# Performance work log

Hardware: AMD Instinct MI355X
Metric: run time of the kernel (lower is better)

Reference implementation:

```python
import jax, jax.numpy as jnp
import numpy as np

D_MODEL = 1024
NHEADS = 16
E_HEAD = D_MODEL // NHEADS  # 64
ROPE_BASE = 10000.0


def _rope_cos_sin(L, dim, base, dtype):
    # dim = E_head (even); inv_freq over pairs, GPT-NeoX half-split convention
    inv_freq = 1.0 / (base ** (jnp.arange(0, dim, 2, dtype=jnp.float32) / dim))
    pos = jnp.arange(L, dtype=jnp.float32)
    freqs = pos[:, None] * inv_freq[None, :]  # [L, dim/2]
    return jnp.cos(freqs).astype(dtype), jnp.sin(freqs).astype(dtype)


def _apply_rope(t, cos, sin):
    # t: [B, H, L, Dh]; rotate-half formulation
    d2 = t.shape[-1] // 2
    t1, t2 = t[..., :d2], t[..., d2:]
    return jnp.concatenate([t1 * cos - t2 * sin, t1 * sin + t2 * cos], axis=-1)


def setup_inputs() -> dict:
    key = jax.random.key(0)
    ks = jax.random.split(key, 5)
    B, L = 4, 2048
    x = jax.random.normal(ks[0], (B, L, D_MODEL), dtype=jnp.float32)
    s_in = 1.0 / np.sqrt(D_MODEL)
    W_packed = jax.random.normal(ks[1], (3 * D_MODEL, D_MODEL), dtype=jnp.float32) * s_in
    b_packed = jax.random.normal(ks[2], (3 * D_MODEL,), dtype=jnp.float32) * 0.02
    W_out = jax.random.normal(ks[3], (D_MODEL, D_MODEL), dtype=jnp.float32) * s_in
    b_out = jax.random.normal(ks[4], (D_MODEL,), dtype=jnp.float32) * 0.02
    return {"x": x, "W_packed": W_packed, "b_packed": b_packed, "W_out": W_out, "b_out": b_out}


def reference(x, W_packed, b_packed, W_out, b_out):
    B, L, _ = x.shape
    # 1) packed QKV projection (query is key is value path)
    qkv = jnp.einsum('ble,fe->blf', x, W_packed) + b_packed  # [B, L, 3*D]
    q, k, v = jnp.split(qkv, 3, axis=-1)
    # 2) split heads -> [B, H, L, Dh]
    def heads(t):
        return t.reshape(B, L, NHEADS, E_HEAD).transpose(0, 2, 1, 3)
    q, k, v = heads(q), heads(k), heads(v)
    # 3) RoPE on q, k
    cos, sin = _rope_cos_sin(L, E_HEAD, ROPE_BASE, x.dtype)
    q = _apply_rope(q, cos, sin)
    k = _apply_rope(k, cos, sin)
    # 4) SDPA (non-causal, no dropout)
    scale = 1.0 / np.sqrt(E_HEAD)
    scores = jnp.einsum('bhqd,bhkd->bhqk', q, k) * scale
    attn = jax.nn.softmax(scores, axis=-1)
    out = jnp.einsum('bhqk,bhkd->bhqd', attn, v)
    # 5) merge heads + output projection
    out = out.transpose(0, 2, 1, 3).reshape(B, L, D_MODEL)
    return jnp.einsum('bld,ed->ble', out, W_out) + b_out
```

## Files before the change

kernel.cpp:

```cpp
#include <hip/hip_runtime.h>
#include <hip/hip_bf16.h>
#include <stdint.h>

#define L_SEQ 2048
#define NB    4
#define NH    16
#define EH    64
#define DM    1024
#define MTOT  (NB * L_SEQ)

typedef __attribute__((ext_vector_type(8))) short bf16x8;
typedef __attribute__((ext_vector_type(4))) float f32x4;
typedef __attribute__((ext_vector_type(16))) float f32x16;

static __device__ __forceinline__ float bf2f(short u) {
    union { unsigned int i; float f; } c;
    c.i = ((unsigned int)(unsigned short)u) << 16;
    return c.f;
}
static __device__ __forceinline__ short f2bf(float f) {
    union { float f; unsigned int i; } c; c.f = f;
    unsigned int x = c.i;
    unsigned int r = (x + 0x7fffu + ((x >> 16) & 1u)) >> 16;
    return (short)(unsigned short)r;
}
static __device__ __forceinline__ unsigned cvtpk(float lo, float hi) {
    unsigned r;
    asm volatile("v_cvt_pk_bf16_f32 %0, %1, %2" : "=v"(r) : "v"(lo), "v"(hi));
    return r;
}

static __device__ __forceinline__ void gload_lds16(const void* g, void* lds) {
    __builtin_amdgcn_global_load_lds(
        (const __attribute__((address_space(1))) unsigned int*)g,
        (__attribute__((address_space(3))) unsigned int*)lds, 16, 0, 0);
}

__global__ __launch_bounds__(256) void cvt3_k(const float* __restrict__ x,
                                              const float* __restrict__ wp,
                                              const float* __restrict__ wo,
                                              short* __restrict__ xb,
                                              short* __restrict__ wpb,
                                              short* __restrict__ wob,
                                              float* __restrict__ tab,
                                              float* __restrict__ tabT) {
    int bid = blockIdx.x;
    if (bid >= 12544) {
        int i = (bid - 12544) * 256 + threadIdx.x;
        int di = i >> 11, l = i & 2047;
        float inv = powf(10000.0f, -(float)di * (1.0f / 32.0f));
        float fr = (float)l * inv;
        tabT[i]         = cosf(fr);
        tabT[65536 + i] = sinf(fr);
        return;
    }
    if (bid >= 12288) {
        int i = (bid - 12288) * 256 + threadIdx.x;
        int l = i >> 5, d = i & 31;
        float inv = powf(10000.0f, -(float)d * (1.0f / 32.0f));
        float fr = (float)l * inv;
        tab[i]         = cosf(fr);
        tab[65536 + i] = sinf(fr);
        return;
    }
    const float* src; short* dst; int i;
    if (bid < 8192)       { src = x;  dst = xb;  i = bid * 256 + threadIdx.x; }
    else if (bid < 11264) { src = wp; dst = wpb; i = (bid - 8192) * 256 + threadIdx.x; }
    else                  { src = wo; dst = wob; i = (bid - 11264) * 256 + threadIdx.x; }
    float4 v = ((const float4*)src)[i];
    short4 o;
    o.x = f2bf(v.x); o.y = f2bf(v.y); o.z = f2bf(v.z); o.w = f2bf(v.w);
    ((short4*)dst)[i] = o;
}

template<int OUTBF16, int NBN, int NCOL, int EPI>
__global__ __launch_bounds__(512, 2) void gemmA_k(const short* __restrict__ A,
                                                  const short* __restrict__ Bt,
                                                  const float* __restrict__ bias,
                                                  void* __restrict__ Cv,
                                                  short* __restrict__ Qp,
                                                  short* __restrict__ Kp,
                                                  short* __restrict__ Vt) {
    __shared__ short lds[2][384 * 32];
    const int t = threadIdx.x;
    const int w = t >> 6, l = t & 63;
    const int wm = w >> 1, wn = w & 1;
    const int lr = l & 15, lh = l >> 4;

    const int nblk = NBN * 32;
    int fid = blockIdx.x + blockIdx.y * NBN;
    int swz = (fid & 7) * (nblk >> 3) + (fid >> 3);
    const int n0 = (swz % NBN) * 128;
    const int m0 = (swz / NBN) * 256;

    const int lrow = l >> 2;
    const int schunk = (l & 3) ^ ((l >> 3) & 3);

    const short* Ag = A + (size_t)(m0 + lrow) * 1024 + schunk * 8;
    const short* Bg = Bt + (size_t)(n0 + lrow) * 1024 + schunk * 8;

    auto STAGE = [&](int kt, int buf) {
        gload_lds16(Ag + (size_t)(w * 32) * 1024 + kt * 32,      &lds[buf][(w * 32) * 32]);
        gload_lds16(Ag + (size_t)(w * 32 + 16) * 1024 + kt * 32, &lds[buf][(w * 32 + 16) * 32]);
        gload_lds16(Bg + (size_t)(w * 16) * 1024 + kt * 32,      &lds[buf][8192 + (w * 16) * 32]);
    };

    f32x4 acc[4][4] = {};

    STAGE(0, 0);
    STAGE(1, 1);
    asm volatile("s_waitcnt vmcnt(3)" ::: "memory");
    __builtin_amdgcn_s_barrier();

    const int fch = (lh ^ ((lr >> 1) & 3)) << 3;

#pragma unroll 2
    for (int kt = 0; kt < 32; ++kt) {
        const int c = kt & 1;
        const short* Al = &lds[c][0];
        const short* Bl = &lds[c][8192];

        bf16x8 bfr[4], af[4];
#pragma unroll
        for (int nj = 0; nj < 4; ++nj)
            bfr[nj] = *(const bf16x8*)(Bl + (wn * 64 + nj * 16 + lr) * 32 + fch);
#pragma unroll
        for (int mi = 0; mi < 4; ++mi)
            af[mi] = *(const bf16x8*)(Al + (wm * 64 + mi * 16 + lr) * 32 + fch);

        __builtin_amdgcn_s_setprio(1);
#pragma unroll
        for (int mi = 0; mi < 4; ++mi)
#pragma unroll
            for (int nj = 0; nj < 4; ++nj)
                acc[mi][nj] = __builtin_amdgcn_mfma_f32_16x16x32_bf16(
                    af[mi], bfr[nj], acc[mi][nj], 0, 0, 0);
        __builtin_amdgcn_s_setprio(0);

        asm volatile("s_waitcnt lgkmcnt(0)" ::: "memory");
        __builtin_amdgcn_s_barrier();
        if (kt + 2 < 32) {
            STAGE(kt + 2, c);
            asm volatile("s_waitcnt vmcnt(3)" ::: "memory");
        } else {
            asm volatile("s_waitcnt vmcnt(0)" ::: "memory");
        }
        __builtin_amdgcn_s_barrier();
    }

    if (EPI == 0) {
#pragma unroll
        for (int mi = 0; mi < 4; ++mi) {
#pragma unroll
            for (int nj = 0; nj < 4; ++nj) {
                const int row = m0 + wm * 64 + mi * 16 + lh * 4;
                const int col = n0 + wn * 64 + nj * 16 + lr;
                const float bsv = bias[col];
#pragma unroll
                for (int j = 0; j < 4; ++j) {
                    float v = acc[mi][nj][j] + bsv;
                    if (OUTBF16)
                        ((short*)Cv)[(size_t)(row + j) * NCOL + col] = f2bf(v);
                    else
                        ((float*)Cv)[(size_t)(row + j) * NCOL + col] = v;
                }
            }
        }
    } else {
        const int part = n0 >> 10;
        const int h = ((n0 & 1023) >> 6) + wn;
#pragma unroll
        for (int mi = 0; mi < 4; ++mi) {
            const int r0 = m0 + wm * 64 + mi * 16 + lh * 4;
            const int bq = r0 >> 11, lq = r0 & 2047;
            if (part < 2) {
                short* Drow = (part == 0 ? Qp : Kp) + ((size_t)(bq * 16 + h) * 2048 + lq) * 64;
#pragma unroll
                for (int nj = 0; nj < 4; ++nj) {
                    const int d = nj * 16 + lr;
                    const float bsv = bias[n0 + wn * 64 + d];
#pragma unroll
                    for (int j = 0; j < 4; ++j)
                        Drow[j * 64 + d] = f2bf(acc[mi][nj][j] + bsv);
                }
            } else {
                const int lpb = (lq & ~63) + (((mi * 2 + (lh & 1)) ^ (lr & 7)) << 3) + ((lh >> 1) * 4);
#pragma unroll
                for (int nj = 0; nj < 4; ++nj) {
                    const int d = nj * 16 + lr;
                    const float bsv = bias[n0 + wn * 64 + d];
                    short4 sv;
                    sv.x = f2bf(acc[mi][nj][0] + bsv);
                    sv.y = f2bf(acc[mi][nj][1] + bsv);
                    sv.z = f2bf(acc[mi][nj][2] + bsv);
                    sv.w = f2bf(acc[mi][nj][3] + bsv);
                    *(short4*)(Vt + (size_t)((bq * 16 + h) * 64 + d) * 2048 + lpb) = sv;
                }
            }
        }
    }
}

__global__ __launch_bounds__(256) void krope_k(const short* __restrict__ Kpre,
                                               const float* __restrict__ tab,
                                               short* __restrict__ Kd) {
    int idx = blockIdx.x * 256 + threadIdx.x;
    int dp = (idx & 7) * 4;
    int h = (idx >> 3) & 15;
    int bl = idx >> 7;
    int l = bl & (L_SEQ - 1);
    int b = bl >> 11;
    float4 cs = *(const float4*)&tab[l * 32 + dp];
    float4 sn = *(const float4*)&tab[65536 + l * 32 + dp];
    size_t ob = ((size_t)((b * 16 + h) * 2048 + l)) * 64;
    const short* src = Kpre + ob;
    short4 k1 = *(const short4*)&src[dp];
    short4 k2 = *(const short4*)&src[dp + 32];
    union { unsigned u[2]; short4 s4; } e1, e2;
    e1.u[0] = cvtpk(bf2f(k1.x) * cs.x - bf2f(k2.x) * sn.x,
                    bf2f(k1.y) * cs.y - bf2f(k2.y) * sn.y);
    e1.u[1] = cvtpk(bf2f(k1.z) * cs.z - bf2f(k2.z) * sn.z,
                    bf2f(k1.w) * cs.w - bf2f(k2.w) * sn.w);
    e2.u[0] = cvtpk(bf2f(k1.x) * sn.x + bf2f(k2.x) * cs.x,
                    bf2f(k1.y) * sn.y + bf2f(k2.y) * cs.y);
    e2.u[1] = cvtpk(bf2f(k1.z) * sn.z + bf2f(k2.z) * cs.z,
                    bf2f(k1.w) * sn.w + bf2f(k2.w) * cs.w);
    int r7 = l & 7;
    int c1 = ((dp >> 3) ^ r7) * 8 + (dp & 7);
    int c2 = (((dp >> 3) | 4) ^ r7) * 8 + (dp & 7);
    *(short4*)(Kd + ob + c1) = e1.s4;
    *(short4*)(Kd + ob + c2) = e2.s4;
}

__global__ __launch_bounds__(512, 2) void attn_k(const short* __restrict__ Qpre,
                                                 const short* __restrict__ Kg,
                                                 const short* __restrict__ Vt,
                                                 const float* __restrict__ tabT,
                                                 short* __restrict__ O) {
    __shared__ short Ks[3][64 * 64];
    __shared__ short Vs[3][64 * 64];
    const int t = threadIdx.x;
    const int w = t >> 6, l = t & 63;
    const int q = l & 31, hi = l >> 5;
    const int r7 = l & 7;

    const int od = blockIdx.x + blockIdx.y * 8;
    const int qblk = (od >> 3) & 7;
    const int bh = (od & 7) * 8 + (od >> 6);
    const int q0 = qblk * 256;

    const short* Kb = Kg + (size_t)bh * (2048 * 64);
    const short* Vb = Vt + (size_t)bh * (64 * 2048);

    const int qrow = q0 + w * 32 + q;

    const short* Qsrc = Qpre + (size_t)bh * (2048 * 64) + (size_t)qrow * 64;
    bf16x8 qraw[4];
#pragma unroll
    for (int ds = 0; ds < 4; ds++)
        qraw[ds] = *(const bf16x8*)(Qsrc + ds * 16 + hi * 8);
    const float sc = 0.18033688011112042f;
    bf16x8 qf[4];
#pragma unroll
    for (int dsL = 0; dsL < 2; dsL++) {
        union { unsigned u[4]; bf16x8 v; } lo, hg;
#pragma unroll
        for (int p = 0; p < 4; p++) {
            const int d0 = dsL * 16 + hi * 8 + 2 * p;
            float c0 = tabT[d0 * 2048 + qrow];
            float s0 = tabT[65536 + d0 * 2048 + qrow];
            float c1 = tabT[(d0 + 1) * 2048 + qrow];
            float s1 = tabT[65536 + (d0 + 1) * 2048 + qrow];
            float a0 = bf2f(qraw[dsL][2 * p]),     b0 = bf2f(qraw[dsL + 2][2 * p]);
            float a1 = bf2f(qraw[dsL][2 * p + 1]), b1 = bf2f(qraw[dsL + 2][2 * p + 1]);
            lo.u[p] = cvtpk((a0 * c0 - b0 * s0) * sc, (a1 * c1 - b1 * s1) * sc);
            hg.u[p] = cvtpk((a0 * s0 + b0 * c0) * sc, (a1 * s1 + b1 * c1) * sc);
        }
        qf[dsL] = lo.v; qf[dsL + 2] = hg.v;
    }

    const short one_bf = (short)0x3F80;
    const bf16x8 ones = {one_bf, one_bf, one_bf, one_bf, one_bf, one_bf, one_bf, one_bf};

    f32x16 o0 = {}, o1 = {}, os = {};

    const int grow = w * 8 + (l >> 3);
    const int gcol = r7 * 8;

    gload_lds16(Kb + (size_t)grow * 64 + gcol,        &Ks[0][w * 512]);
    gload_lds16(Vb + (size_t)grow * 2048 + gcol,      &Vs[0][w * 512]);
    gload_lds16(Kb + (size_t)(64 + grow) * 64 + gcol, &Ks[1][w * 512]);
    gload_lds16(Vb + (size_t)grow * 2048 + 64 + gcol, &Vs[1][w * 512]);
    asm volatile("s_waitcnt vmcnt(2)" ::: "memory");
    __builtin_amdgcn_s_barrier();

    const short* Kc = &Ks[0][0];  const short* Vc = &Vs[0][0];
    const short* Kn = &Ks[1][0];  const short* Vn = &Vs[1][0];
    short*       Kf = &Ks[2][0];  short*       Vf = &Vs[2][0];

    for (int it = 0; it < 32; ++it) {
        if (it < 30) {
            const int kn = (it + 2) * 64;
            gload_lds16(Kb + (size_t)(kn + grow) * 64 + gcol, Kf + w * 512);
            gload_lds16(Vb + (size_t)grow * 2048 + kn + gcol, Vf + w * 512);
        }

        f32x16 s0 = {}, s1 = {};
#pragma unroll
        for (int ds = 0; ds < 4; ds++) {
            const int ch = ((ds << 1) | hi) ^ r7;
            bf16x8 k0f = *(const bf16x8*)(Kc + q * 64 + ch * 8);
            bf16x8 k1f = *(const bf16x8*)(Kc + (32 + q) * 64 + ch * 8);
            __builtin_amdgcn_s_setprio(1);
            s0 = __builtin_amdgcn_mfma_f32_32x32x16_bf16(k0f, qf[ds], s0, 0, 0, 0);
            s1 = __builtin_amdgcn_mfma_f32_32x32x16_bf16(k1f, qf[ds], s1, 0, 0, 0);
            __builtin_amdgcn_s_setprio(0);
        }

#pragma unroll
        for (int r = 0; r < 16; r++) {
            s0[r] = __builtin_amdgcn_exp2f(s0[r]);
            s1[r] = __builtin_amdgcn_exp2f(s1[r]);
        }

        bf16x8 pf[4];
        {
            union { unsigned u[4]; bf16x8 v; } f;
            f.u[0] = cvtpk(s0[0], s0[1]);  f.u[1] = cvtpk(s0[2], s0[3]);
            f.u[2] = cvtpk(s0[4], s0[5]);  f.u[3] = cvtpk(s0[6], s0[7]);
            pf[0] = f.v;
            f.u[0] = cvtpk(s0[8], s0[9]);  f.u[1] = cvtpk(s0[10], s0[11]);
            f.u[2] = cvtpk(s0[12], s0[13]); f.u[3] = cvtpk(s0[14], s0[15]);
            pf[1] = f.v;
            f.u[0] = cvtpk(s1[0], s1[1]);  f.u[1] = cvtpk(s1[2], s1[3]);
            f.u[2] = cvtpk(s1[4], s1[5]);  f.u[3] = cvtpk(s1[6], s1[7]);
            pf[2] = f.v;
            f.u[0] = cvtpk(s1[8], s1[9]);  f.u[1] = cvtpk(s1[10], s1[11]);
            f.u[2] = cvtpk(s1[12], s1[13]); f.u[3] = cvtpk(s1[14], s1[15]);
            pf[3] = f.v;
        }

#pragma unroll
        for (int ks = 0; ks < 4; ks++) {
            const int ch = ((ks << 1) | hi) ^ r7;
            bf16x8 v0f = *(const bf16x8*)(Vc + q * 64 + ch * 8);
            bf16x8 v1f = *(const bf16x8*)(Vc + (32 + q) * 64 + ch * 8);
            __builtin_amdgcn_s_setprio(1);
            o0 = __builtin_amdgcn_mfma_f32_32x32x16_bf16(v0f, pf[ks], o0, 0, 0, 0);
            o1 = __builtin_amdgcn_mfma_f32_32x32x16_bf16(v1f, pf[ks], o1, 0, 0, 0);
            os = __builtin_amdgcn_mfma_f32_32x32x16_bf16(ones, pf[ks], os, 0, 0, 0);
            __builtin_amdgcn_s_setprio(0);
        }

        asm volatile("s_waitcnt lgkmcnt(0)" ::: "memory");
        if (it < 30) asm volatile("s_waitcnt vmcnt(2)" ::: "memory");
        else         asm volatile("s_waitcnt vmcnt(0)" ::: "memory");
        __builtin_amdgcn_s_barrier();

        const short* tk = Kc; Kc = Kn; Kn = Kf; Kf = (short*)tk;
        const short* tv = Vc; Vc = Vn; Vn = Vf; Vf = (short*)tv;
    }

    const float inv = 1.0f / os[0];
    const int b = bh >> 4, h = bh & 15;
    short* Orow = O + (size_t)(b * 2048 + qrow) * 1024 + h * 64;
#pragma unroll
    for (int g = 0; g < 4; g++) {
        unsigned w0 = cvtpk(o0[g * 4 + 0] * inv, o0[g * 4 + 1] * inv);
        unsigned w1 = cvtpk(o0[g * 4 + 2] * inv, o0[g * 4 + 3] * inv);
        unsigned long long p0 = (unsigned long long)w0 | ((unsigned long long)w1 << 32);
        *(unsigned long long*)(Orow + g * 8 + hi * 4) = p0;
        unsigned w2 = cvtpk(o1[g * 4 + 0] * inv, o1[g * 4 + 1] * inv);
        unsigned w3 = cvtpk(o1[g * 4 + 2] * inv, o1[g * 4 + 3] * inv);
        unsigned long long p1 = (unsigned long long)w2 | ((unsigned long long)w3 << 32);
        *(unsigned long long*)(Orow + 32 + g * 8 + hi * 4) = p1;
    }
}

extern "C" void kernel_launch(void* const* d_in, const int* in_sizes, int n_in,
                              void* d_out, int out_size, void* d_ws, size_t ws_size,
                              hipStream_t stream) {
    const float* x  = (const float*)d_in[0];
    const float* Wp = (const float*)d_in[1];
    const float* bp = (const float*)d_in[2];
    const float* Wo = (const float*)d_in[3];
    const float* bo = (const float*)d_in[4];

    char* ws = (char*)d_ws;
    const size_t SZ_XB  = (size_t)MTOT * DM * 2;
    const size_t SZ_WPB = (size_t)3 * DM * DM * 2;
    const size_t SZ_WOB = (size_t)DM * DM * 2;
    const size_t SZ_BHLE = (size_t)MTOT * DM * 2;
    const size_t SZ_TAB = (size_t)131072 * 4;

    short* xb   = (short*)(ws);
    short* wpb  = (short*)(ws + SZ_XB);
    short* wob  = (short*)(ws + SZ_XB + SZ_WPB);
    short* Qpre = (short*)(ws + SZ_XB + SZ_WPB + SZ_WOB);
    short* Kpre = (short*)(ws + SZ_XB + SZ_WPB + SZ_WOB + SZ_BHLE);
    short* Kb   = (short*)(ws + SZ_XB + SZ_WPB + SZ_WOB + 2 * SZ_BHLE);
    short* Vtb  = (short*)(ws + SZ_XB + SZ_WPB + SZ_WOB + 3 * SZ_BHLE);
    short* Ob   = (short*)(ws + SZ_XB + SZ_WPB + SZ_WOB + 4 * SZ_BHLE);
    float* tab  = (float*)(ws + SZ_XB + SZ_WPB + SZ_WOB + 5 * SZ_BHLE);
    float* tabT = (float*)(ws + SZ_XB + SZ_WPB + SZ_WOB + 5 * SZ_BHLE + SZ_TAB);

    cvt3_k<<<12800, 256, 0, stream>>>(x, Wp, Wo, xb, wpb, wob, tab, tabT);

    gemmA_k<1, 24, 3072, 1><<<dim3(24, 32), 512, 0, stream>>>(
        xb, wpb, bp, nullptr, Qpre, Kpre, Vtb);

    krope_k<<<4096, 256, 0, stream>>>(Kpre, tab, Kb);

    attn_k<<<dim3(8, 64), 512, 0, stream>>>(Qpre, Kb, Vtb, tabT, Ob);

    gemmA_k<0, 8, 1024, 0><<<dim3(8, 32), 512, 0, stream>>>(
        Ob, wob, bo, (float*)d_out, nullptr, nullptr, nullptr);
}
```

Before: 185.5 us.

## Triple-buffer GEMM LDS with one barrier per k-step; drop transposed RoPE table

The GEMM mainloop moves from two to three LDS buffers. The next-next tile is now issued at the start of each iteration, so only one barrier per k-step is needed instead of two, giving loads more time to overlap with the MFMAs. Separately, the transposed cos/sin table is removed and attention reads the row-major table with vectorized float4 loads instead of strided scalar loads, which also shrinks the conversion kernel's grid. The cost is 50% more LDS per GEMM block, which may limit occupancy at 2 blocks per CU.

```diff
diff --git a/kernel.cpp b/kernel.cpp
--- a/kernel.cpp
+++ b/kernel.cpp
@@ -42,18 +42,8 @@
                                               short* __restrict__ xb,
                                               short* __restrict__ wpb,
                                               short* __restrict__ wob,
-                                              float* __restrict__ tab,
-                                              float* __restrict__ tabT) {
+                                              float* __restrict__ tab) {
     int bid = blockIdx.x;
-    if (bid >= 12544) {
-        int i = (bid - 12544) * 256 + threadIdx.x;
-        int di = i >> 11, l = i & 2047;
-        float inv = powf(10000.0f, -(float)di * (1.0f / 32.0f));
-        float fr = (float)l * inv;
-        tabT[i]         = cosf(fr);
-        tabT[65536 + i] = sinf(fr);
-        return;
-    }
     if (bid >= 12288) {
         int i = (bid - 12288) * 256 + threadIdx.x;
         int l = i >> 5, d = i & 31;
@@ -81,7 +71,7 @@
                                                   short* __restrict__ Qp,
                                                   short* __restrict__ Kp,
                                                   short* __restrict__ Vt) {
-    __shared__ short lds[2][384 * 32];
+    __shared__ short lds[3][384 * 32];
     const int t = threadIdx.x;
     const int w = t >> 6, l = t & 63;
     const int wm = w >> 1, wn = w & 1;
@@ -99,26 +89,30 @@
     const short* Ag = A + (size_t)(m0 + lrow) * 1024 + schunk * 8;
     const short* Bg = Bt + (size_t)(n0 + lrow) * 1024 + schunk * 8;
 
-    auto STAGE = [&](int kt, int buf) {
-        gload_lds16(Ag + (size_t)(w * 32) * 1024 + kt * 32,      &lds[buf][(w * 32) * 32]);
-        gload_lds16(Ag + (size_t)(w * 32 + 16) * 1024 + kt * 32, &lds[buf][(w * 32 + 16) * 32]);
-        gload_lds16(Bg + (size_t)(w * 16) * 1024 + kt * 32,      &lds[buf][8192 + (w * 16) * 32]);
+    auto STAGE = [&](int kt, short* dst) {
+        gload_lds16(Ag + (size_t)(w * 32) * 1024 + kt * 32,      dst + (w * 32) * 32);
+        gload_lds16(Ag + (size_t)(w * 32 + 16) * 1024 + kt * 32, dst + (w * 32 + 16) * 32);
+        gload_lds16(Bg + (size_t)(w * 16) * 1024 + kt * 32,      dst + 8192 + (w * 16) * 32);
     };
 
     f32x4 acc[4][4] = {};
 
-    STAGE(0, 0);
-    STAGE(1, 1);
+    STAGE(0, &lds[0][0]);
+    STAGE(1, &lds[1][0]);
     asm volatile("s_waitcnt vmcnt(3)" ::: "memory");
     __builtin_amdgcn_s_barrier();
 
+    short* Pc = &lds[0][0];
+    short* Pn = &lds[1][0];
+    short* Pf = &lds[2][0];
+
     const int fch = (lh ^ ((lr >> 1) & 3)) << 3;
 
-#pragma unroll 2
     for (int kt = 0; kt < 32; ++kt) {
-        const int c = kt & 1;
-        const short* Al = &lds[c][0];
-        const short* Bl = &lds[c][8192];
+        if (kt < 30) STAGE(kt + 2, Pf);
+
+        const short* Al = Pc;
+        const short* Bl = Pc + 8192;
 
         bf16x8 bfr[4], af[4];
 #pragma unroll
@@ -138,14 +132,11 @@
         __builtin_amdgcn_s_setprio(0);
 
         asm volatile("s_waitcnt lgkmcnt(0)" ::: "memory");
+        if (kt < 30) asm volatile("s_waitcnt vmcnt(3)" ::: "memory");
+        else         asm volatile("s_waitcnt vmcnt(0)" ::: "memory");
         __builtin_amdgcn_s_barrier();
-        if (kt + 2 < 32) {
-            STAGE(kt + 2, c);
-            asm volatile("s_waitcnt vmcnt(3)" ::: "memory");
-        } else {
-            asm volatile("s_waitcnt vmcnt(0)" ::: "memory");
-        }
-        __builtin_amdgcn_s_barrier();
+
+        short* tp = Pc; Pc = Pn; Pn = Pf; Pf = tp;
     }
 
     if (EPI == 0) {
@@ -235,7 +226,7 @@
 __global__ __launch_bounds__(512, 2) void attn_k(const short* __restrict__ Qpre,
                                                  const short* __restrict__ Kg,
                                                  const short* __restrict__ Vt,
-                                                 const float* __restrict__ tabT,
+                                                 const float* __restrict__ tab,
                                                  short* __restrict__ O) {
     __shared__ short Ks[3][64 * 64];
     __shared__ short Vs[3][64 * 64];
@@ -263,18 +254,22 @@
     bf16x8 qf[4];
 #pragma unroll
     for (int dsL = 0; dsL < 2; dsL++) {
+        const float* tc = tab + qrow * 32 + dsL * 16 + hi * 8;
+        float4 ca = *(const float4*)tc;
+        float4 cb = *(const float4*)(tc + 4);
+        float4 sa = *(const float4*)(tc + 65536);
+        float4 sb = *(const float4*)(tc + 65536 + 4);
+        const float cv[8] = {ca.x, ca.y, ca.z, ca.w, cb.x, cb.y, cb.z, cb.w};
+        const float sv[8] = {sa.x, sa.y, sa.z, sa.w, sb.x, sb.y, sb.z, sb.w};
         union { unsigned u[4]; bf16x8 v; } lo, hg;
 #pragma unroll
         for (int p = 0; p < 4; p++) {
-            const int d0 = dsL * 16 + hi * 8 + 2 * p;
-            float c0 = tabT[d0 * 2048 + qrow];
-            float s0 = tabT[65536 + d0 * 2048 + qrow];
-            float c1 = tabT[(d0 + 1) * 2048 + qrow];
-            float s1 = tabT[65536 + (d0 + 1) * 2048 + qrow];
             float a0 = bf2f(qraw[dsL][2 * p]),     b0 = bf2f(qraw[dsL + 2][2 * p]);
             float a1 = bf2f(qraw[dsL][2 * p + 1]), b1 = bf2f(qraw[dsL + 2][2 * p + 1]);
-            lo.u[p] = cvtpk((a0 * c0 - b0 * s0) * sc, (a1 * c1 - b1 * s1) * sc);
-            hg.u[p] = cvtpk((a0 * s0 + b0 * c0) * sc, (a1 * s1 + b1 * c1) * sc);
+            lo.u[p] = cvtpk((a0 * cv[2 * p] - b0 * sv[2 * p]) * sc,
+                            (a1 * cv[2 * p + 1] - b1 * sv[2 * p + 1]) * sc);
+            hg.u[p] = cvtpk((a0 * sv[2 * p] + b0 * cv[2 * p]) * sc,
+                            (a1 * sv[2 * p + 1] + b1 * cv[2 * p + 1]) * sc);
         }
         qf[dsL] = lo.v; qf[dsL + 2] = hg.v;
     }
@@ -391,7 +386,6 @@
     const size_t SZ_WPB = (size_t)3 * DM * DM * 2;
     const size_t SZ_WOB = (size_t)DM * DM * 2;
     const size_t SZ_BHLE = (size_t)MTOT * DM * 2;
-    const size_t SZ_TAB = (size_t)131072 * 4;
 
     short* xb   = (short*)(ws);
     short* wpb  = (short*)(ws + SZ_XB);
@@ -402,16 +396,15 @@
     short* Vtb  = (short*)(ws + SZ_XB + SZ_WPB + SZ_WOB + 3 * SZ_BHLE);
     short* Ob   = (short*)(ws + SZ_XB + SZ_WPB + SZ_WOB + 4 * SZ_BHLE);
     float* tab  = (float*)(ws + SZ_XB + SZ_WPB + SZ_WOB + 5 * SZ_BHLE);
-    float* tabT = (float*)(ws + SZ_XB + SZ_WPB + SZ_WOB + 5 * SZ_BHLE + SZ_TAB);
-
-    cvt3_k<<<12800, 256, 0, stream>>>(x, Wp, Wo, xb, wpb, wob, tab, tabT);
+
+    cvt3_k<<<12544, 256, 0, stream>>>(x, Wp, Wo, xb, wpb, wob, tab);
 
     gemmA_k<1, 24, 3072, 1><<<dim3(24, 32), 512, 0, stream>>>(
         xb, wpb, bp, nullptr, Qpre, Kpre, Vtb);
 
     krope_k<<<4096, 256, 0, stream>>>(Kpre, tab, Kb);
 
-    attn_k<<<dim3(8, 64), 512, 0, stream>>>(Qpre, Kb, Vtb, tabT, Ob);
+    attn_k<<<dim3(8, 64), 512, 0, stream>>>(Qpre, Kb, Vtb, tab, Ob);
 
     gemmA_k<0, 8, 1024, 0><<<dim3(8, 32), 512, 0, stream>>>(
         Ob, wob, bo, (float*)d_out, nullptr, nullptr, nullptr);
```

Measured after the change: 183.1 us. No clear change (-1.3%).
